# Kernel optimization log

Hardware: AMD Instinct MI355X
Metric: run time of the kernel (lower is better)

## Reference

```python
import jax, jax.numpy as jnp
import numpy as np

E = 100000   # num edges
N = 50000    # num nodes (eg_idx, v, t triples)
B = 64       # num queries / subgraphs
D = 128      # n_dims_in
ID = 4 * D   # concat of 4 embeddings
OD = 2 * D   # G output dims
K = 1000     # max_edges per eg_idx


def setup_inputs() -> dict:
    key = jax.random.key(0)
    ks = jax.random.split(key, 12)
    eg_idx = jnp.sort(jax.random.randint(ks[0], (E,), 0, B)).astype(jnp.int32)
    node_i = jax.random.randint(ks[1], (E,), 0, N).astype(jnp.int32)
    node_j = jax.random.randint(ks[2], (E,), 0, N).astype(jnp.int32)
    node_score = jax.random.uniform(ks[3], (N,), dtype=jnp.float32)
    memorized_embedding = jax.random.normal(ks[4], (N, D), dtype=jnp.float32)
    rel_emb = jax.random.normal(ks[5], (E, D), dtype=jnp.float32)
    query_src_ts_emb = jax.random.normal(ks[6], (B, D), dtype=jnp.float32)
    query_rel_emb = jax.random.normal(ks[7], (B, D), dtype=jnp.float32)
    # G params: left/right dense init ~ N(0, sqrt(2/in)), center xavier-ish
    Wl = jax.random.normal(ks[8], (ID, OD), dtype=jnp.float32) * np.sqrt(2.0 / ID)
    Wr = jax.random.normal(ks[9], (ID, OD), dtype=jnp.float32) * np.sqrt(2.0 / ID)
    Wc = jax.random.normal(ks[10], (OD, OD), dtype=jnp.float32) * np.sqrt(2.0 / (OD + OD))
    bl = jnp.zeros((OD,), jnp.float32)
    br = jnp.zeros((OD,), jnp.float32)
    bc = jnp.zeros((OD,), jnp.float32)
    return dict(eg_idx=eg_idx, node_i=node_i, node_j=node_j, node_score=node_score,
                memorized_embedding=memorized_embedding, rel_emb=rel_emb,
                query_src_ts_emb=query_src_ts_emb, query_rel_emb=query_rel_emb,
                Wl=Wl, bl=bl, Wr=Wr, br=br, Wc=Wc, bc=bc, k=K)


def _segment_softmax(logits, seg, num_segments):
    m = jax.ops.segment_max(logits, seg, num_segments=num_segments)
    e = jnp.exp(logits - m[seg])
    s = jax.ops.segment_sum(e, seg, num_segments=num_segments)
    return e / s[seg]


def _topk_keep_mask(scores, group, num_groups, k):
    # keep edge iff its score ranks < k within its group (per-eg_idx topk)
    n = scores.shape[0]
    order = jnp.lexsort((-scores, group))          # sort by group asc, score desc
    sorted_group = group[order]
    counts = jax.ops.segment_sum(jnp.ones((n,), jnp.int32), group, num_segments=num_groups)
    starts = jnp.cumsum(counts) - counts           # exclusive cumsum: group start offsets
    rank_in_group = jnp.arange(n) - starts[sorted_group]
    keep_sorted = rank_in_group < k
    return jnp.zeros((n,), bool).at[order].set(keep_sorted)


def reference(eg_idx, node_i, node_j, node_score, memorized_embedding, rel_emb,
              query_src_ts_emb, query_rel_emb, Wl, bl, Wr, br, Wc, bc, k):
    num_nodes = memorized_embedding.shape[0]
    num_groups = query_src_ts_emb.shape[0]
    # gather per-edge embeddings
    hvi = memorized_embedding[node_i]              # [E, D]
    hvj = memorized_embedding[node_j]
    q_src = query_src_ts_emb[eg_idx]               # [E, D]
    q_rel = query_rel_emb[eg_idx]
    # G: bilinear MLP attention
    left_x = jnp.concatenate([hvi, rel_emb, q_src, q_rel], axis=-1)   # [E, 4D]
    right_x = jnp.concatenate([hvj, rel_emb, q_src, q_rel], axis=-1)
    l = jax.nn.leaky_relu(left_x @ Wl + bl)                           # [E, 2D]
    r = jax.nn.leaky_relu(right_x @ Wr + br) @ Wc + bc
    transition_logits = jnp.sum(l * r, axis=-1)                       # [E]
    # segment softmax over source node (eg_idx, vi, ti)
    soft = _segment_softmax(transition_logits, node_i, num_nodes)
    src_att = node_score[node_i]
    target_att = soft * src_att
    # per-eg_idx top-k pruning (keep mask instead of ragged slicing)
    keep = _topk_keep_mask(target_att, eg_idx, num_groups, k).astype(target_att.dtype)
    # sum aggregation: scatter soft * target_att into target nodes over kept edges
    updated_node_score = jax.ops.segment_sum(keep * soft * target_att, node_j,
                                             num_segments=num_nodes)
    return updated_node_score
```

## Files before the change

### kernel.cpp

```cpp
#include <hip/hip_runtime.h>

#define DD   128
#define ODIM 256
#define TE   32
#define TSLICE 16

__device__ __forceinline__ float leaky(float v) { return v > 0.f ? v : 0.01f * v; }

__global__ void k_query(const float* __restrict__ qs, const float* __restrict__ qr,
                        const float* __restrict__ Wl, const float* __restrict__ bl,
                        const float* __restrict__ Wr, const float* __restrict__ br,
                        float* __restrict__ Ql, float* __restrict__ Qr)
{
    const int g = blockIdx.x, t = threadIdx.x;
    float al = bl[t], ar = br[t];
    const float* qsg = qs + (size_t)g * DD;
    const float* qrg = qr + (size_t)g * DD;
    for (int k = 0; k < DD; ++k) {
        float a = qsg[k], b = qrg[k];
        al = fmaf(a, Wl[(size_t)(256 + k) * ODIM + t], al);
        al = fmaf(b, Wl[(size_t)(384 + k) * ODIM + t], al);
        ar = fmaf(a, Wr[(size_t)(256 + k) * ODIM + t], ar);
        ar = fmaf(b, Wr[(size_t)(384 + k) * ODIM + t], ar);
    }
    Ql[(size_t)g * ODIM + t] = al;
    Qr[(size_t)g * ODIM + t] = ar;
}

#define FMA4(dst, xc, wv, j)                                \
    dst[j][0] = fmaf(xc, wv.x, dst[j][0]);                  \
    dst[j][1] = fmaf(xc, wv.y, dst[j][1]);                  \
    dst[j][2] = fmaf(xc, wv.z, dst[j][2]);                  \
    dst[j][3] = fmaf(xc, wv.w, dst[j][3]);

__global__ __launch_bounds__(256, 2)
void k_nodepre(const float* __restrict__ me, const float* __restrict__ Wl,
               const float* __restrict__ Wr, float* __restrict__ Xl,
               float* __restrict__ Xr, int N)
{
    __shared__ float s_me[TE][DD];

    const int tx = threadIdx.x;
    const int cg = tx & 63;
    const int er = tx >> 6;
    const int c0 = cg << 2;
    const int n0 = blockIdx.x * TE;
    const int eb = er * 8;

    for (int it = tx; it < TE * DD / 4; it += 256) {
        int i  = it >> 5;
        int kk = (it & 31) << 2;
        float4 h = make_float4(0.f, 0.f, 0.f, 0.f);
        if (n0 + i < N) h = *(const float4*)(me + (size_t)(n0 + i) * DD + kk);
        *(float4*)(&s_me[i][kk]) = h;
    }
    __syncthreads();

    float acc[8][4];
#pragma unroll
    for (int j = 0; j < 8; ++j) { acc[j][0] = acc[j][1] = acc[j][2] = acc[j][3] = 0.f; }
#pragma unroll 2
    for (int k = 0; k < DD; k += 4) {
        const float* wp = Wl + (size_t)k * ODIM + c0;
        float4 w0 = *(const float4*)(wp);
        float4 w1 = *(const float4*)(wp + ODIM);
        float4 w2 = *(const float4*)(wp + 2 * ODIM);
        float4 w3 = *(const float4*)(wp + 3 * ODIM);
#pragma unroll
        for (int j = 0; j < 8; ++j) {
            float4 x = *(const float4*)(&s_me[eb + j][k]);
            FMA4(acc, x.x, w0, j) FMA4(acc, x.y, w1, j) FMA4(acc, x.z, w2, j) FMA4(acc, x.w, w3, j)
        }
    }
#pragma unroll
    for (int j = 0; j < 8; ++j) {
        int n = n0 + eb + j;
        if (n < N)
            *(float4*)(Xl + (size_t)n * ODIM + c0) = make_float4(acc[j][0], acc[j][1], acc[j][2], acc[j][3]);
    }

#pragma unroll
    for (int j = 0; j < 8; ++j) { acc[j][0] = acc[j][1] = acc[j][2] = acc[j][3] = 0.f; }
#pragma unroll 2
    for (int k = 0; k < DD; k += 4) {
        const float* wp = Wr + (size_t)k * ODIM + c0;
        float4 w0 = *(const float4*)(wp);
        float4 w1 = *(const float4*)(wp + ODIM);
        float4 w2 = *(const float4*)(wp + 2 * ODIM);
        float4 w3 = *(const float4*)(wp + 3 * ODIM);
#pragma unroll
        for (int j = 0; j < 8; ++j) {
            float4 x = *(const float4*)(&s_me[eb + j][k]);
            FMA4(acc, x.x, w0, j) FMA4(acc, x.y, w1, j) FMA4(acc, x.z, w2, j) FMA4(acc, x.w, w3, j)
        }
    }
#pragma unroll
    for (int j = 0; j < 8; ++j) {
        int n = n0 + eb + j;
        if (n < N)
            *(float4*)(Xr + (size_t)n * ODIM + c0) = make_float4(acc[j][0], acc[j][1], acc[j][2], acc[j][3]);
    }
}

__global__ __launch_bounds__(256, 2)
void k_edge_logits_pre(const int* __restrict__ eg_idx, const int* __restrict__ node_i,
                       const int* __restrict__ node_j, const float* __restrict__ rel,
                       const float* __restrict__ Wl, const float* __restrict__ Wr,
                       const float* __restrict__ Wc, const float* __restrict__ bc,
                       const float* __restrict__ Ql, const float* __restrict__ Qr,
                       const float* __restrict__ Xl, const float* __restrict__ Xr,
                       float* __restrict__ logits, int E)
{
    __shared__ float s_a[TE][DD];
    __shared__ float s_b[TE][DD];
    __shared__ int   s_ni[TE], s_nj[TE], s_g[TE];

    const int tx = threadIdx.x;
    const int cg = tx & 63;
    const int er = tx >> 6;
    const int c0 = cg << 2;
    const int e0 = blockIdx.x * TE;
    const int eb = er * 8;

    if (tx < TE) {
        int e = e0 + tx;
        s_ni[tx] = (e < E) ? node_i[e] : 0;
        s_nj[tx] = (e < E) ? node_j[e] : 0;
        s_g[tx]  = (e < E) ? eg_idx[e] : 0;
    }
    __syncthreads();

    for (int it = tx; it < TE * DD / 4; it += 256) {
        int i  = it >> 5;
        int kk = (it & 31) << 2;
        float4 v = make_float4(0.f, 0.f, 0.f, 0.f);
        if (e0 + i < E) v = *(const float4*)(rel + (size_t)(e0 + i) * DD + kk);
        *(float4*)(&s_a[i][kk]) = v;
    }
    __syncthreads();

    float acc[8][4];
#pragma unroll
    for (int j = 0; j < 8; ++j) { acc[j][0] = acc[j][1] = acc[j][2] = acc[j][3] = 0.f; }

#pragma unroll 2
    for (int k = 0; k < DD; k += 4) {
        const float* wp = Wr + (size_t)(DD + k) * ODIM + c0;
        float4 w0 = *(const float4*)(wp);
        float4 w1 = *(const float4*)(wp + ODIM);
        float4 w2 = *(const float4*)(wp + 2 * ODIM);
        float4 w3 = *(const float4*)(wp + 3 * ODIM);
#pragma unroll
        for (int j = 0; j < 8; ++j) {
            float4 x = *(const float4*)(&s_a[eb + j][k]);
            FMA4(acc, x.x, w0, j) FMA4(acc, x.y, w1, j) FMA4(acc, x.z, w2, j) FMA4(acc, x.w, w3, j)
        }
    }

#pragma unroll
    for (int j = 0; j < 8; ++j) {
        float4 xr = *(const float4*)(Xr + (size_t)s_nj[eb + j] * ODIM + c0);
        float4 q  = *(const float4*)(Qr + (size_t)s_g[eb + j] * ODIM + c0);
        acc[j][0] = leaky(acc[j][0] + xr.x + q.x);
        acc[j][1] = leaky(acc[j][1] + xr.y + q.y);
        acc[j][2] = leaky(acc[j][2] + xr.z + q.z);
        acc[j][3] = leaky(acc[j][3] + xr.w + q.w);
    }

    float uacc[8][4];
#pragma unroll
    for (int j = 0; j < 8; ++j) { uacc[j][0] = uacc[j][1] = uacc[j][2] = uacc[j][3] = 0.f; }

    if (c0 < DD) {
#pragma unroll
        for (int j = 0; j < 8; ++j)
            *(float4*)(&s_b[eb + j][c0]) = make_float4(acc[j][0], acc[j][1], acc[j][2], acc[j][3]);
    }
    __syncthreads();
#pragma unroll 2
    for (int k = 0; k < DD; k += 4) {
        const float* wp = Wc + (size_t)k * ODIM + c0;
        float4 w0 = *(const float4*)(wp);
        float4 w1 = *(const float4*)(wp + ODIM);
        float4 w2 = *(const float4*)(wp + 2 * ODIM);
        float4 w3 = *(const float4*)(wp + 3 * ODIM);
#pragma unroll
        for (int j = 0; j < 8; ++j) {
            float4 x = *(const float4*)(&s_b[eb + j][k]);
            FMA4(uacc, x.x, w0, j) FMA4(uacc, x.y, w1, j) FMA4(uacc, x.z, w2, j) FMA4(uacc, x.w, w3, j)
        }
    }
    __syncthreads();
    if (c0 >= DD) {
#pragma unroll
        for (int j = 0; j < 8; ++j)
            *(float4*)(&s_b[eb + j][c0 - DD]) = make_float4(acc[j][0], acc[j][1], acc[j][2], acc[j][3]);
    }
    __syncthreads();
#pragma unroll 2
    for (int k = 0; k < DD; k += 4) {
        const float* wp = Wc + (size_t)(DD + k) * ODIM + c0;
        float4 w0 = *(const float4*)(wp);
        float4 w1 = *(const float4*)(wp + ODIM);
        float4 w2 = *(const float4*)(wp + 2 * ODIM);
        float4 w3 = *(const float4*)(wp + 3 * ODIM);
#pragma unroll
        for (int j = 0; j < 8; ++j) {
            float4 x = *(const float4*)(&s_b[eb + j][k]);
            FMA4(uacc, x.x, w0, j) FMA4(uacc, x.y, w1, j) FMA4(uacc, x.z, w2, j) FMA4(uacc, x.w, w3, j)
        }
    }

    {
        float4 bcv = *(const float4*)(bc + c0);
#pragma unroll
        for (int j = 0; j < 8; ++j) {
            uacc[j][0] += bcv.x; uacc[j][1] += bcv.y;
            uacc[j][2] += bcv.z; uacc[j][3] += bcv.w;
        }
    }

#pragma unroll
    for (int j = 0; j < 8; ++j) { acc[j][0] = acc[j][1] = acc[j][2] = acc[j][3] = 0.f; }
#pragma unroll 2
    for (int k = 0; k < DD; k += 4) {
        const float* wp = Wl + (size_t)(DD + k) * ODIM + c0;
        float4 w0 = *(const float4*)(wp);
        float4 w1 = *(const float4*)(wp + ODIM);
        float4 w2 = *(const float4*)(wp + 2 * ODIM);
        float4 w3 = *(const float4*)(wp + 3 * ODIM);
#pragma unroll
        for (int j = 0; j < 8; ++j) {
            float4 x = *(const float4*)(&s_a[eb + j][k]);
            FMA4(acc, x.x, w0, j) FMA4(acc, x.y, w1, j) FMA4(acc, x.z, w2, j) FMA4(acc, x.w, w3, j)
        }
    }

#pragma unroll
    for (int j = 0; j < 8; ++j) {
        float4 xl = *(const float4*)(Xl + (size_t)s_ni[eb + j] * ODIM + c0);
        float4 q  = *(const float4*)(Ql + (size_t)s_g[eb + j] * ODIM + c0);
        float p = leaky(acc[j][0] + xl.x + q.x) * uacc[j][0]
                + leaky(acc[j][1] + xl.y + q.y) * uacc[j][1]
                + leaky(acc[j][2] + xl.z + q.z) * uacc[j][2]
                + leaky(acc[j][3] + xl.w + q.w) * uacc[j][3];
#pragma unroll
        for (int off = 32; off > 0; off >>= 1) p += __shfl_down(p, off);
        if (cg == 0) {
            int e = e0 + eb + j;
            if (e < E) logits[e] = p;
        }
    }
}

__global__ __launch_bounds__(256, 2)
void k_edge_logits(const int* __restrict__ eg_idx, const int* __restrict__ node_i,
                   const int* __restrict__ node_j,
                   const float* __restrict__ me, const float* __restrict__ rel,
                   const float* __restrict__ Wl, const float* __restrict__ Wr,
                   const float* __restrict__ Wc, const float* __restrict__ bc,
                   const float* __restrict__ Ql, const float* __restrict__ Qr,
                   float* __restrict__ logits, int E)
{
    __shared__ float s_a[TE][DD];
    __shared__ float s_b[TE][DD];
    __shared__ int   s_ni[TE], s_nj[TE], s_g[TE];

    const int tx = threadIdx.x;
    const int cg = tx & 63;
    const int er = tx >> 6;
    const int c0 = cg << 2;
    const int e0 = blockIdx.x * TE;
    const int eb = er * 8;

    if (tx < TE) {
        int e = e0 + tx;
        s_ni[tx] = (e < E) ? node_i[e] : 0;
        s_nj[tx] = (e < E) ? node_j[e] : 0;
        s_g[tx]  = (e < E) ? eg_idx[e] : 0;
    }
    __syncthreads();

    for (int it = tx; it < TE * DD / 4; it += 256) {
        int i  = it >> 5;
        int kk = (it & 31) << 2;
        float4 v = make_float4(0.f, 0.f, 0.f, 0.f);
        float4 h = v;
        if (e0 + i < E) {
            v = *(const float4*)(rel + (size_t)(e0 + i) * DD + kk);
            h = *(const float4*)(me + (size_t)s_nj[i] * DD + kk);
        }
        *(float4*)(&s_a[i][kk]) = v;
        *(float4*)(&s_b[i][kk]) = h;
    }
    __syncthreads();

    float acc[8][4];
#pragma unroll
    for (int j = 0; j < 8; ++j) { acc[j][0] = acc[j][1] = acc[j][2] = acc[j][3] = 0.f; }

    for (int k = 0; k < DD; k += 4) {
        const float* wp = Wr + (size_t)k * ODIM + c0;
        float4 w0 = *(const float4*)(wp);
        float4 w1 = *(const float4*)(wp + ODIM);
        float4 w2 = *(const float4*)(wp + 2 * ODIM);
        float4 w3 = *(const float4*)(wp + 3 * ODIM);
#pragma unroll
        for (int j = 0; j < 8; ++j) {
            float4 x = *(const float4*)(&s_b[eb + j][k]);
            FMA4(acc, x.x, w0, j) FMA4(acc, x.y, w1, j) FMA4(acc, x.z, w2, j) FMA4(acc, x.w, w3, j)
        }
    }
    for (int k = 0; k < DD; k += 4) {
        const float* wp = Wr + (size_t)(DD + k) * ODIM + c0;
        float4 w0 = *(const float4*)(wp);
        float4 w1 = *(const float4*)(wp + ODIM);
        float4 w2 = *(const float4*)(wp + 2 * ODIM);
        float4 w3 = *(const float4*)(wp + 3 * ODIM);
#pragma unroll
        for (int j = 0; j < 8; ++j) {
            float4 x = *(const float4*)(&s_a[eb + j][k]);
            FMA4(acc, x.x, w0, j) FMA4(acc, x.y, w1, j) FMA4(acc, x.z, w2, j) FMA4(acc, x.w, w3, j)
        }
    }

#pragma unroll
    for (int j = 0; j < 8; ++j) {
        int g = s_g[eb + j];
        float4 q = *(const float4*)(Qr + (size_t)g * ODIM + c0);
        acc[j][0] = leaky(acc[j][0] + q.x);
        acc[j][1] = leaky(acc[j][1] + q.y);
        acc[j][2] = leaky(acc[j][2] + q.z);
        acc[j][3] = leaky(acc[j][3] + q.w);
    }

    float uacc[8][4];
#pragma unroll
    for (int j = 0; j < 8; ++j) { uacc[j][0] = uacc[j][1] = uacc[j][2] = uacc[j][3] = 0.f; }

    __syncthreads();
    if (c0 < DD) {
#pragma unroll
        for (int j = 0; j < 8; ++j)
            *(float4*)(&s_b[eb + j][c0]) = make_float4(acc[j][0], acc[j][1], acc[j][2], acc[j][3]);
    }
    __syncthreads();
    for (int k = 0; k < DD; k += 4) {
        const float* wp = Wc + (size_t)k * ODIM + c0;
        float4 w0 = *(const float4*)(wp);
        float4 w1 = *(const float4*)(wp + ODIM);
        float4 w2 = *(const float4*)(wp + 2 * ODIM);
        float4 w3 = *(const float4*)(wp + 3 * ODIM);
#pragma unroll
        for (int j = 0; j < 8; ++j) {
            float4 x = *(const float4*)(&s_b[eb + j][k]);
            FMA4(uacc, x.x, w0, j) FMA4(uacc, x.y, w1, j) FMA4(uacc, x.z, w2, j) FMA4(uacc, x.w, w3, j)
        }
    }
    __syncthreads();
    if (c0 >= DD) {
#pragma unroll
        for (int j = 0; j < 8; ++j)
            *(float4*)(&s_b[eb + j][c0 - DD]) = make_float4(acc[j][0], acc[j][1], acc[j][2], acc[j][3]);
    }
    __syncthreads();
    for (int k = 0; k < DD; k += 4) {
        const float* wp = Wc + (size_t)(DD + k) * ODIM + c0;
        float4 w0 = *(const float4*)(wp);
        float4 w1 = *(const float4*)(wp + ODIM);
        float4 w2 = *(const float4*)(wp + 2 * ODIM);
        float4 w3 = *(const float4*)(wp + 3 * ODIM);
#pragma unroll
        for (int j = 0; j < 8; ++j) {
            float4 x = *(const float4*)(&s_b[eb + j][k]);
            FMA4(uacc, x.x, w0, j) FMA4(uacc, x.y, w1, j) FMA4(uacc, x.z, w2, j) FMA4(uacc, x.w, w3, j)
        }
    }

    {
        float4 bcv = *(const float4*)(bc + c0);
#pragma unroll
        for (int j = 0; j < 8; ++j) {
            uacc[j][0] += bcv.x; uacc[j][1] += bcv.y;
            uacc[j][2] += bcv.z; uacc[j][3] += bcv.w;
        }
    }

    __syncthreads();
    for (int it = tx; it < TE * DD / 4; it += 256) {
        int i  = it >> 5;
        int kk = (it & 31) << 2;
        float4 h = make_float4(0.f, 0.f, 0.f, 0.f);
        if (e0 + i < E) h = *(const float4*)(me + (size_t)s_ni[i] * DD + kk);
        *(float4*)(&s_b[i][kk]) = h;
    }
    __syncthreads();

#pragma unroll
    for (int j = 0; j < 8; ++j) { acc[j][0] = acc[j][1] = acc[j][2] = acc[j][3] = 0.f; }

    for (int k = 0; k < DD; k += 4) {
        const float* wp = Wl + (size_t)k * ODIM + c0;
        float4 w0 = *(const float4*)(wp);
        float4 w1 = *(const float4*)(wp + ODIM);
        float4 w2 = *(const float4*)(wp + 2 * ODIM);
        float4 w3 = *(const float4*)(wp + 3 * ODIM);
#pragma unroll
        for (int j = 0; j < 8; ++j) {
            float4 x = *(const float4*)(&s_b[eb + j][k]);
            FMA4(acc, x.x, w0, j) FMA4(acc, x.y, w1, j) FMA4(acc, x.z, w2, j) FMA4(acc, x.w, w3, j)
        }
    }
    for (int k = 0; k < DD; k += 4) {
        const float* wp = Wl + (size_t)(DD + k) * ODIM + c0;
        float4 w0 = *(const float4*)(wp);
        float4 w1 = *(const float4*)(wp + ODIM);
        float4 w2 = *(const float4*)(wp + 2 * ODIM);
        float4 w3 = *(const float4*)(wp + 3 * ODIM);
#pragma unroll
        for (int j = 0; j < 8; ++j) {
            float4 x = *(const float4*)(&s_a[eb + j][k]);
            FMA4(acc, x.x, w0, j) FMA4(acc, x.y, w1, j) FMA4(acc, x.z, w2, j) FMA4(acc, x.w, w3, j)
        }
    }

#pragma unroll
    for (int j = 0; j < 8; ++j) {
        int g = s_g[eb + j];
        float4 q = *(const float4*)(Ql + (size_t)g * ODIM + c0);
        float p = leaky(acc[j][0] + q.x) * uacc[j][0]
                + leaky(acc[j][1] + q.y) * uacc[j][1]
                + leaky(acc[j][2] + q.z) * uacc[j][2]
                + leaky(acc[j][3] + q.w) * uacc[j][3];
#pragma unroll
        for (int off = 32; off > 0; off >>= 1) p += __shfl_down(p, off);
        if (cg == 0) {
            int e = e0 + eb + j;
            if (e < E) logits[e] = p;
        }
    }
}

__device__ __forceinline__ unsigned f32_enc(float f) {
    unsigned u = __float_as_uint(f);
    return (u & 0x80000000u) ? ~u : (u | 0x80000000u);
}
__device__ __forceinline__ float f32_dec(unsigned x) {
    return (x & 0x80000000u) ? __uint_as_float(x & 0x7fffffffu) : __uint_as_float(~x);
}

__global__ void k_segmax(const float* __restrict__ logits, const int* __restrict__ ni,
                         unsigned* __restrict__ segmax, int E)
{
    int e = blockIdx.x * 256 + threadIdx.x;
    if (e >= E) return;
    atomicMax(&segmax[ni[e]], f32_enc(logits[e]));
}

__global__ void k_expsum(const float* __restrict__ logits, const int* __restrict__ ni,
                         const unsigned* __restrict__ segmax,
                         float* __restrict__ eexp, float* __restrict__ segsum, int E)
{
    int e = blockIdx.x * 256 + threadIdx.x;
    if (e >= E) return;
    float m = f32_dec(segmax[ni[e]]);
    float v = expf(logits[e] - m);
    eexp[e] = v;
    atomicAdd(&segsum[ni[e]], v);
}

__global__ void k_soft(const float* __restrict__ eexp, const float* __restrict__ segsum,
                       const int* __restrict__ ni, const float* __restrict__ node_score,
                       float* __restrict__ soft, float* __restrict__ ta, int E)
{
    int e = blockIdx.x * 256 + threadIdx.x;
    if (e >= E) return;
    int n = ni[e];
    float s = eexp[e] / segsum[n];
    soft[e] = s;
    ta[e]   = s * node_score[n];
}

__global__ void k_starts(const int* __restrict__ eg, int E, int B, int* __restrict__ starts)
{
    int g = blockIdx.x * blockDim.x + threadIdx.x;
    if (g > B) return;
    int lo = 0, hi = E;
    while (lo < hi) { int mid = (lo + hi) >> 1; if (eg[mid] < g) lo = mid + 1; else hi = mid; }
    starts[g] = lo;
}

__global__ __launch_bounds__(256)
void k_topk(const int* __restrict__ starts, const int* __restrict__ node_j,
            const float* __restrict__ soft, const float* __restrict__ ta,
            const int* __restrict__ kptr, float* __restrict__ out)
{
    __shared__ float s_val[2048];
    const int g  = blockIdx.x / TSLICE;
    const int sl = blockIdx.x % TSLICE;
    const int gs = starts[g], ge = starts[g + 1];
    const int cnt = ge - gs;
    if (cnt <= 0) return;
    const int per = (cnt + TSLICE - 1) / TSLICE;
    const int c0  = sl * per;
    const int c1  = min(cnt, c0 + per);
    if (c0 >= cnt) return;
    const int K  = kptr[0];
    const int tx = threadIdx.x;

    for (int base = c0; base < c1; base += 256) {
        int   li  = base + tx;
        bool  act = li < c1;
        float mv  = act ? ta[gs + li] : 0.f;
        int   rank = 0;
        for (int t0 = 0; t0 < cnt; t0 += 2048) {
            int tlen = min(2048, cnt - t0);
            __syncthreads();
            for (int i = tx; i < tlen; i += 256) s_val[i] = ta[gs + t0 + i];
            __syncthreads();
            for (int i = 0; i < tlen; ++i) {
                float v  = s_val[i];
                int   gi = t0 + i;
                rank += (int)((v > mv) || (v == mv && gi < li));
            }
        }
        if (act && rank < K) {
            int e = gs + li;
            atomicAdd(&out[node_j[e]], soft[e] * ta[e]);
        }
    }
}

extern "C" void kernel_launch(void* const* d_in, const int* in_sizes, int n_in,
                              void* d_out, int out_size, void* d_ws, size_t ws_size,
                              hipStream_t stream)
{
    const int*   eg_idx     = (const int*)d_in[0];
    const int*   node_i     = (const int*)d_in[1];
    const int*   node_j     = (const int*)d_in[2];
    const float* node_score = (const float*)d_in[3];
    const float* me         = (const float*)d_in[4];
    const float* rel        = (const float*)d_in[5];
    const float* qs         = (const float*)d_in[6];
    const float* qr         = (const float*)d_in[7];
    const float* Wl         = (const float*)d_in[8];
    const float* bl         = (const float*)d_in[9];
    const float* Wr         = (const float*)d_in[10];
    const float* br         = (const float*)d_in[11];
    const float* Wc         = (const float*)d_in[12];
    const float* bc         = (const float*)d_in[13];
    const int*   kptr       = (const int*)d_in[14];

    const int E = in_sizes[0];
    const int N = in_sizes[3];
    const int B = in_sizes[6] / DD;

    float* ws      = (float*)d_ws;
    float* logits  = ws;
    float* eexp    = ws + (size_t)E;
    float* soft    = ws + 2 * (size_t)E;
    float* ta      = ws + 3 * (size_t)E;
    unsigned* segmax = (unsigned*)(ws + 4 * (size_t)E);
    float* segsum  = ws + 4 * (size_t)E + (size_t)N;
    float* Ql      = ws + 4 * (size_t)E + 2 * (size_t)N;
    float* Qr      = Ql + (size_t)B * ODIM;
    int*   starts  = (int*)(Qr + (size_t)B * ODIM);
    size_t base    = 4 * (size_t)E + 2 * (size_t)N + 2 * (size_t)B * ODIM + (size_t)(B + 1);
    float* Xl      = ws + base;
    float* Xr      = Xl + (size_t)N * ODIM;
    size_t needed  = (base + 2 * (size_t)N * ODIM) * sizeof(float);
    bool use_pre   = ws_size >= needed;

    hipMemsetAsync(d_out, 0, (size_t)N * sizeof(float), stream);
    hipMemsetAsync(segmax, 0, (size_t)2 * N * sizeof(float), stream);

    k_query<<<B, 256, 0, stream>>>(qs, qr, Wl, bl, Wr, br, Ql, Qr);
    if (use_pre) {
        k_nodepre<<<(N + TE - 1) / TE, 256, 0, stream>>>(me, Wl, Wr, Xl, Xr, N);
        k_edge_logits_pre<<<(E + TE - 1) / TE, 256, 0, stream>>>(eg_idx, node_i, node_j, rel,
                                                                 Wl, Wr, Wc, bc, Ql, Qr,
                                                                 Xl, Xr, logits, E);
    } else {
        k_edge_logits<<<(E + TE - 1) / TE, 256, 0, stream>>>(eg_idx, node_i, node_j, me, rel,
                                                             Wl, Wr, Wc, bc, Ql, Qr, logits, E);
    }
    int gE = (E + 255) / 256;
    k_segmax<<<gE, 256, 0, stream>>>(logits, node_i, segmax, E);
    k_expsum<<<gE, 256, 0, stream>>>(logits, node_i, segmax, eexp, segsum, E);
    k_soft<<<gE, 256, 0, stream>>>(eexp, segsum, node_i, node_score, soft, ta, E);
    k_starts<<<1, 128, 0, stream>>>(eg_idx, E, B, starts);
    k_topk<<<B * TSLICE, 256, 0, stream>>>(starts, node_j, soft, ta, kptr, (float*)d_out);
}
```

Before: 630.0 us.

## Remap threads so each wave owns a column slice across all tile edges

Changes the thread-to-work mapping in the node-precompute and edge-logit GEMM kernels. Each wave now covers a 64-column slice for all 32 edges instead of all 256 columns for 8 edges, so weight float4 loads per wave shrink and LDS reads of the activation tile become more broadcast-friendly. The per-edge dot-product reduction now uses a 16-lane xor shuffle plus a small shared-memory cross-wave sum. The partial unroll pragmas are also removed. The trade-off is an extra barrier and LDS buffer, and a possible change in register pressure.

```diff
diff --git a/kernel.cpp b/kernel.cpp
--- a/kernel.cpp
+++ b/kernel.cpp
@@ -33,6 +33,7 @@
     dst[j][2] = fmaf(xc, wv.z, dst[j][2]);                  \
     dst[j][3] = fmaf(xc, wv.w, dst[j][3]);
 
+
 __global__ __launch_bounds__(256, 2)
 void k_nodepre(const float* __restrict__ me, const float* __restrict__ Wl,
                const float* __restrict__ Wr, float* __restrict__ Xl,
@@ -40,12 +41,14 @@
 {
     __shared__ float s_me[TE][DD];
 
-    const int tx = threadIdx.x;
-    const int cg = tx & 63;
-    const int er = tx >> 6;
-    const int c0 = cg << 2;
-    const int n0 = blockIdx.x * TE;
-    const int eb = er * 8;
+    const int tx   = threadIdx.x;
+    const int wave = tx >> 6;
+    const int lane = tx & 63;
+    const int colg = lane & 15;
+    const int edgeg= lane >> 4;
+    const int c0   = wave * 64 + colg * 4;
+    const int eb   = edgeg * 8;
+    const int n0   = blockIdx.x * TE;
 
     for (int it = tx; it < TE * DD / 4; it += 256) {
         int i  = it >> 5;
@@ -59,7 +62,6 @@
     float acc[8][4];
 #pragma unroll
     for (int j = 0; j < 8; ++j) { acc[j][0] = acc[j][1] = acc[j][2] = acc[j][3] = 0.f; }
-#pragma unroll 2
     for (int k = 0; k < DD; k += 4) {
         const float* wp = Wl + (size_t)k * ODIM + c0;
         float4 w0 = *(const float4*)(wp);
@@ -81,7 +83,6 @@
 
 #pragma unroll
     for (int j = 0; j < 8; ++j) { acc[j][0] = acc[j][1] = acc[j][2] = acc[j][3] = 0.f; }
-#pragma unroll 2
     for (int k = 0; k < DD; k += 4) {
         const float* wp = Wr + (size_t)k * ODIM + c0;
         float4 w0 = *(const float4*)(wp);
@@ -113,14 +114,17 @@
 {
     __shared__ float s_a[TE][DD];
     __shared__ float s_b[TE][DD];
+    __shared__ float s_red[4][TE];
     __shared__ int   s_ni[TE], s_nj[TE], s_g[TE];
 
-    const int tx = threadIdx.x;
-    const int cg = tx & 63;
-    const int er = tx >> 6;
-    const int c0 = cg << 2;
-    const int e0 = blockIdx.x * TE;
-    const int eb = er * 8;
+    const int tx   = threadIdx.x;
+    const int wave = tx >> 6;
+    const int lane = tx & 63;
+    const int colg = lane & 15;
+    const int edgeg= lane >> 4;
+    const int c0   = wave * 64 + colg * 4;
+    const int eb   = edgeg * 8;
+    const int e0   = blockIdx.x * TE;
 
     if (tx < TE) {
         int e = e0 + tx;
@@ -143,7 +147,6 @@
 #pragma unroll
     for (int j = 0; j < 8; ++j) { acc[j][0] = acc[j][1] = acc[j][2] = acc[j][3] = 0.f; }
 
-#pragma unroll 2
     for (int k = 0; k < DD; k += 4) {
         const float* wp = Wr + (size_t)(DD + k) * ODIM + c0;
         float4 w0 = *(const float4*)(wp);
@@ -171,13 +174,12 @@
 #pragma unroll
     for (int j = 0; j < 8; ++j) { uacc[j][0] = uacc[j][1] = uacc[j][2] = uacc[j][3] = 0.f; }
 
-    if (c0 < DD) {
+    if (wave < 2) {
 #pragma unroll
         for (int j = 0; j < 8; ++j)
             *(float4*)(&s_b[eb + j][c0]) = make_float4(acc[j][0], acc[j][1], acc[j][2], acc[j][3]);
     }
     __syncthreads();
-#pragma unroll 2
     for (int k = 0; k < DD; k += 4) {
         const float* wp = Wc + (size_t)k * ODIM + c0;
         float4 w0 = *(const float4*)(wp);
@@ -191,13 +193,12 @@
         }
     }
     __syncthreads();
-    if (c0 >= DD) {
+    if (wave >= 2) {
 #pragma unroll
         for (int j = 0; j < 8; ++j)
             *(float4*)(&s_b[eb + j][c0 - DD]) = make_float4(acc[j][0], acc[j][1], acc[j][2], acc[j][3]);
     }
     __syncthreads();
-#pragma unroll 2
     for (int k = 0; k < DD; k += 4) {
         const float* wp = Wc + (size_t)(DD + k) * ODIM + c0;
         float4 w0 = *(const float4*)(wp);
@@ -222,7 +223,6 @@
 
 #pragma unroll
     for (int j = 0; j < 8; ++j) { acc[j][0] = acc[j][1] = acc[j][2] = acc[j][3] = 0.f; }
-#pragma unroll 2
     for (int k = 0; k < DD; k += 4) {
         const float* wp = Wl + (size_t)(DD + k) * ODIM + c0;
         float4 w0 = *(const float4*)(wp);
@@ -244,12 +244,17 @@
                 + leaky(acc[j][1] + xl.y + q.y) * uacc[j][1]
                 + leaky(acc[j][2] + xl.z + q.z) * uacc[j][2]
                 + leaky(acc[j][3] + xl.w + q.w) * uacc[j][3];
-#pragma unroll
-        for (int off = 32; off > 0; off >>= 1) p += __shfl_down(p, off);
-        if (cg == 0) {
-            int e = e0 + eb + j;
-            if (e < E) logits[e] = p;
-        }
+        p += __shfl_xor(p, 1);
+        p += __shfl_xor(p, 2);
+        p += __shfl_xor(p, 4);
+        p += __shfl_xor(p, 8);
+        if (colg == 0) s_red[wave][eb + j] = p;
+    }
+    __syncthreads();
+    if (tx < TE) {
+        int e = e0 + tx;
+        if (e < E)
+            logits[e] = s_red[0][tx] + s_red[1][tx] + s_red[2][tx] + s_red[3][tx];
     }
 }
 
```

Measured after the change: 581.3 us. 7.7% less time.

## Double-buffer weight chunks into LDS via async global_load_lds in GEMM kernels

Applied to the files above, without the earlier changes.

Instead of each thread reading weight float4s straight from global memory inside the k-loop, weights are staged in 8-row chunks into a double-buffered LDS tile using __builtin_amdgcn_global_load_lds. The next chunk is prefetched while the current one is consumed, with one barrier per chunk. This targets global-load latency and redundant per-wave weight fetches in the node-precompute and edge-logit kernels. The cost is extra LDS (16 KB), a __syncthreads per chunk, and reliance on the barrier to cover async LDS-write completion. The fallback kernel only has TE replaced by the literal 32.

```diff
diff --git a/kernel.cpp b/kernel.cpp
--- a/kernel.cpp
+++ b/kernel.cpp
@@ -1,9 +1,13 @@
 #include <hip/hip_runtime.h>
 
-#define DD   128
-#define ODIM 256
-#define TE   32
+#define DD     128
+#define ODIM   256
+#define TE     32
+#define WCHUNK 8
 #define TSLICE 16
+
+#define GLOBAL_AS __attribute__((address_space(1)))
+#define LDS_AS    __attribute__((address_space(3)))
 
 __device__ __forceinline__ float leaky(float v) { return v > 0.f ? v : 0.01f * v; }
 
@@ -33,19 +37,54 @@
     dst[j][2] = fmaf(xc, wv.z, dst[j][2]);                  \
     dst[j][3] = fmaf(xc, wv.w, dst[j][3]);
 
+#define GEMM_CHUNK(XS, DST)                                              \
+    {                                                                    \
+        _Pragma("unroll")                                                \
+        for (int kk = 0; kk < 2; ++kk) {                                 \
+            const int k = cbase + kk * 4;                                \
+            float4 w0 = *(const float4*)(&s_w[buf][kk * 4 + 0][c0]);     \
+            float4 w1 = *(const float4*)(&s_w[buf][kk * 4 + 1][c0]);     \
+            float4 w2 = *(const float4*)(&s_w[buf][kk * 4 + 2][c0]);     \
+            float4 w3 = *(const float4*)(&s_w[buf][kk * 4 + 3][c0]);     \
+            _Pragma("unroll")                                            \
+            for (int j = 0; j < 8; ++j) {                                \
+                float4 x = *(const float4*)(&XS[eb + j][k]);             \
+                FMA4(DST, x.x, w0, j) FMA4(DST, x.y, w1, j)              \
+                FMA4(DST, x.z, w2, j) FMA4(DST, x.w, w3, j)              \
+            }                                                            \
+        }                                                                \
+    }
+
 __global__ __launch_bounds__(256, 2)
 void k_nodepre(const float* __restrict__ me, const float* __restrict__ Wl,
                const float* __restrict__ Wr, float* __restrict__ Xl,
                float* __restrict__ Xr, int N)
 {
     __shared__ float s_me[TE][DD];
-
-    const int tx = threadIdx.x;
-    const int cg = tx & 63;
-    const int er = tx >> 6;
-    const int c0 = cg << 2;
-    const int n0 = blockIdx.x * TE;
-    const int eb = er * 8;
+    __shared__ float s_w[2][WCHUNK][ODIM];
+
+    const int tx   = threadIdx.x;
+    const int cg   = tx & 63;
+    const int er   = tx >> 6;
+    const int lane = cg;
+    const int c0   = cg << 2;
+    const int eb   = er * 8;
+    const int n0   = blockIdx.x * TE;
+
+    auto wseq = [&](int c) -> const float* {
+        return (c < 16) ? (Wl + (size_t)(8 * c) * ODIM)
+                        : (Wr + (size_t)(8 * (c - 16)) * ODIM);
+    };
+    auto stage_w = [&](const float* base, int nb) {
+#pragma unroll
+        for (int q = 0; q < 2; ++q) {
+            int off = er * 512 + q * 256 + lane * 4;
+            __builtin_amdgcn_global_load_lds(
+                (const GLOBAL_AS void*)(base + off),
+                (LDS_AS void*)(&s_w[nb][0][0] + off),
+                16, 0, 0);
+        }
+    };
 
     for (int it = tx; it < TE * DD / 4; it += 256) {
         int i  = it >> 5;
@@ -54,23 +93,20 @@
         if (n0 + i < N) h = *(const float4*)(me + (size_t)(n0 + i) * DD + kk);
         *(float4*)(&s_me[i][kk]) = h;
     }
+    stage_w(wseq(0), 0);
     __syncthreads();
 
     float acc[8][4];
 #pragma unroll
     for (int j = 0; j < 8; ++j) { acc[j][0] = acc[j][1] = acc[j][2] = acc[j][3] = 0.f; }
-#pragma unroll 2
-    for (int k = 0; k < DD; k += 4) {
-        const float* wp = Wl + (size_t)k * ODIM + c0;
-        float4 w0 = *(const float4*)(wp);
-        float4 w1 = *(const float4*)(wp + ODIM);
-        float4 w2 = *(const float4*)(wp + 2 * ODIM);
-        float4 w3 = *(const float4*)(wp + 3 * ODIM);
-#pragma unroll
-        for (int j = 0; j < 8; ++j) {
-            float4 x = *(const float4*)(&s_me[eb + j][k]);
-            FMA4(acc, x.x, w0, j) FMA4(acc, x.y, w1, j) FMA4(acc, x.z, w2, j) FMA4(acc, x.w, w3, j)
-        }
+    int buf = 0;
+
+    for (int c = 0; c < 16; ++c) {
+        stage_w(wseq(c + 1), buf ^ 1);
+        const int cbase = c * 8;
+        GEMM_CHUNK(s_me, acc)
+        __syncthreads();
+        buf ^= 1;
     }
 #pragma unroll
     for (int j = 0; j < 8; ++j) {
@@ -81,18 +117,13 @@
 
 #pragma unroll
     for (int j = 0; j < 8; ++j) { acc[j][0] = acc[j][1] = acc[j][2] = acc[j][3] = 0.f; }
-#pragma unroll 2
-    for (int k = 0; k < DD; k += 4) {
-        const float* wp = Wr + (size_t)k * ODIM + c0;
-        float4 w0 = *(const float4*)(wp);
-        float4 w1 = *(const float4*)(wp + ODIM);
-        float4 w2 = *(const float4*)(wp + 2 * ODIM);
-        float4 w3 = *(const float4*)(wp + 3 * ODIM);
-#pragma unroll
-        for (int j = 0; j < 8; ++j) {
-            float4 x = *(const float4*)(&s_me[eb + j][k]);
-            FMA4(acc, x.x, w0, j) FMA4(acc, x.y, w1, j) FMA4(acc, x.z, w2, j) FMA4(acc, x.w, w3, j)
-        }
+
+    for (int c = 16; c < 32; ++c) {
+        if (c < 31) stage_w(wseq(c + 1), buf ^ 1);
+        const int cbase = (c - 16) * 8;
+        GEMM_CHUNK(s_me, acc)
+        __syncthreads();
+        buf ^= 1;
     }
 #pragma unroll
     for (int j = 0; j < 8; ++j) {
@@ -113,14 +144,33 @@
 {
     __shared__ float s_a[TE][DD];
     __shared__ float s_b[TE][DD];
+    __shared__ float s_w[2][WCHUNK][ODIM];
     __shared__ int   s_ni[TE], s_nj[TE], s_g[TE];
 
-    const int tx = threadIdx.x;
-    const int cg = tx & 63;
-    const int er = tx >> 6;
-    const int c0 = cg << 2;
-    const int e0 = blockIdx.x * TE;
-    const int eb = er * 8;
+    const int tx   = threadIdx.x;
+    const int cg   = tx & 63;
+    const int er   = tx >> 6;
+    const int lane = cg;
+    const int c0   = cg << 2;
+    const int e0   = blockIdx.x * TE;
+    const int eb   = er * 8;
+
+    auto wseq = [&](int c) -> const float* {
+        if (c < 16) return Wr + (size_t)(DD + 8 * c) * ODIM;
+        if (c < 32) return Wc + (size_t)(8 * (c - 16)) * ODIM;
+        if (c < 48) return Wc + (size_t)(DD + 8 * (c - 32)) * ODIM;
+        return Wl + (size_t)(DD + 8 * (c - 48)) * ODIM;
+    };
+    auto stage_w = [&](const float* base, int nb) {
+#pragma unroll
+        for (int q = 0; q < 2; ++q) {
+            int off = er * 512 + q * 256 + lane * 4;
+            __builtin_amdgcn_global_load_lds(
+                (const GLOBAL_AS void*)(base + off),
+                (LDS_AS void*)(&s_w[nb][0][0] + off),
+                16, 0, 0);
+        }
+    };
 
     if (tx < TE) {
         int e = e0 + tx;
@@ -128,7 +178,6 @@
         s_nj[tx] = (e < E) ? node_j[e] : 0;
         s_g[tx]  = (e < E) ? eg_idx[e] : 0;
     }
-    __syncthreads();
 
     for (int it = tx; it < TE * DD / 4; it += 256) {
         int i  = it >> 5;
@@ -137,24 +186,20 @@
         if (e0 + i < E) v = *(const float4*)(rel + (size_t)(e0 + i) * DD + kk);
         *(float4*)(&s_a[i][kk]) = v;
     }
+    stage_w(wseq(0), 0);
     __syncthreads();
 
     float acc[8][4];
 #pragma unroll
     for (int j = 0; j < 8; ++j) { acc[j][0] = acc[j][1] = acc[j][2] = acc[j][3] = 0.f; }
-
-#pragma unroll 2
-    for (int k = 0; k < DD; k += 4) {
-        const float* wp = Wr + (size_t)(DD + k) * ODIM + c0;
-        float4 w0 = *(const float4*)(wp);
-        float4 w1 = *(const float4*)(wp + ODIM);
-        float4 w2 = *(const float4*)(wp + 2 * ODIM);
-        float4 w3 = *(const float4*)(wp + 3 * ODIM);
-#pragma unroll
-        for (int j = 0; j < 8; ++j) {
-            float4 x = *(const float4*)(&s_a[eb + j][k]);
-            FMA4(acc, x.x, w0, j) FMA4(acc, x.y, w1, j) FMA4(acc, x.z, w2, j) FMA4(acc, x.w, w3, j)
-        }
+    int buf = 0;
+
+    for (int c = 0; c < 16; ++c) {
+        stage_w(wseq(c + 1), buf ^ 1);
+        const int cbase = c * 8;
+        GEMM_CHUNK(s_a, acc)
+        __syncthreads();
+        buf ^= 1;
     }
 
 #pragma unroll
@@ -177,38 +222,28 @@
             *(float4*)(&s_b[eb + j][c0]) = make_float4(acc[j][0], acc[j][1], acc[j][2], acc[j][3]);
     }
     __syncthreads();
-#pragma unroll 2
-    for (int k = 0; k < DD; k += 4) {
-        const float* wp = Wc + (size_t)k * ODIM + c0;
-        float4 w0 = *(const float4*)(wp);
-        float4 w1 = *(const float4*)(wp + ODIM);
-        float4 w2 = *(const float4*)(wp + 2 * ODIM);
-        float4 w3 = *(const float4*)(wp + 3 * ODIM);
-#pragma unroll
-        for (int j = 0; j < 8; ++j) {
-            float4 x = *(const float4*)(&s_b[eb + j][k]);
-            FMA4(uacc, x.x, w0, j) FMA4(uacc, x.y, w1, j) FMA4(uacc, x.z, w2, j) FMA4(uacc, x.w, w3, j)
-        }
-    }
-    __syncthreads();
+
+    for (int c = 16; c < 32; ++c) {
+        stage_w(wseq(c + 1), buf ^ 1);
+        const int cbase = (c - 16) * 8;
+        GEMM_CHUNK(s_b, uacc)
+        __syncthreads();
+        buf ^= 1;
+    }
+
     if (c0 >= DD) {
 #pragma unroll
         for (int j = 0; j < 8; ++j)
             *(float4*)(&s_b[eb + j][c0 - DD]) = make_float4(acc[j][0], acc[j][1], acc[j][2], acc[j][3]);
     }
     __syncthreads();
-#pragma unroll 2
-    for (int k = 0; k < DD; k += 4) {
-        const float* wp = Wc + (size_t)(DD + k) * ODIM + c0;
-        float4 w0 = *(const float4*)(wp);
-        float4 w1 = *(const float4*)(wp + ODIM);
-        float4 w2 = *(const float4*)(wp + 2 * ODIM);
-        float4 w3 = *(const float4*)(wp + 3 * ODIM);
-#pragma unroll
-        for (int j = 0; j < 8; ++j) {
-            float4 x = *(const float4*)(&s_b[eb + j][k]);
-            FMA4(uacc, x.x, w0, j) FMA4(uacc, x.y, w1, j) FMA4(uacc, x.z, w2, j) FMA4(uacc, x.w, w3, j)
-        }
+
+    for (int c = 32; c < 48; ++c) {
+        stage_w(wseq(c + 1), buf ^ 1);
+        const int cbase = (c - 32) * 8;
+        GEMM_CHUNK(s_b, uacc)
+        __syncthreads();
+        buf ^= 1;
     }
 
     {
@@ -222,18 +257,12 @@
 
 #pragma unroll
     for (int j = 0; j < 8; ++j) { acc[j][0] = acc[j][1] = acc[j][2] = acc[j][3] = 0.f; }
-#pragma unroll 2
-    for (int k = 0; k < DD; k += 4) {
-        const float* wp = Wl + (size_t)(DD + k) * ODIM + c0;
-        float4 w0 = *(const float4*)(wp);
-        float4 w1 = *(const float4*)(wp + ODIM);
-        float4 w2 = *(const float4*)(wp + 2 * ODIM);
-        float4 w3 = *(const float4*)(wp + 3 * ODIM);
-#pragma unroll
-        for (int j = 0; j < 8; ++j) {
-            float4 x = *(const float4*)(&s_a[eb + j][k]);
-            FMA4(acc, x.x, w0, j) FMA4(acc, x.y, w1, j) FMA4(acc, x.z, w2, j) FMA4(acc, x.w, w3, j)
-        }
+    for (int c = 48; c < 64; ++c) {
+        if (c < 63) stage_w(wseq(c + 1), buf ^ 1);
+        const int cbase = (c - 48) * 8;
+        GEMM_CHUNK(s_a, acc)
+        __syncthreads();
+        buf ^= 1;
     }
 
 #pragma unroll
@@ -262,18 +291,18 @@
                    const float* __restrict__ Ql, const float* __restrict__ Qr,
                    float* __restrict__ logits, int E)
 {
-    __shared__ float s_a[TE][DD];
-    __shared__ float s_b[TE][DD];
-    __shared__ int   s_ni[TE], s_nj[TE], s_g[TE];
+    __shared__ float s_a[32][DD];
+    __shared__ float s_b[32][DD];
+    __shared__ int   s_ni[32], s_nj[32], s_g[32];
 
     const int tx = threadIdx.x;
     const int cg = tx & 63;
     const int er = tx >> 6;
     const int c0 = cg << 2;
-    const int e0 = blockIdx.x * TE;
+    const int e0 = blockIdx.x * 32;
     const int eb = er * 8;
 
-    if (tx < TE) {
+    if (tx < 32) {
         int e = e0 + tx;
         s_ni[tx] = (e < E) ? node_i[e] : 0;
         s_nj[tx] = (e < E) ? node_j[e] : 0;
@@ -281,7 +310,7 @@
     }
     __syncthreads();
 
-    for (int it = tx; it < TE * DD / 4; it += 256) {
+    for (int it = tx; it < 32 * DD / 4; it += 256) {
         int i  = it >> 5;
         int kk = (it & 31) << 2;
         float4 v = make_float4(0.f, 0.f, 0.f, 0.f);
@@ -387,7 +416,7 @@
     }
 
     __syncthreads();
-    for (int it = tx; it < TE * DD / 4; it += 256) {
+    for (int it = tx; it < 32 * DD / 4; it += 256) {
         int i  = it >> 5;
         int kk = (it & 31) << 2;
         float4 h = make_float4(0.f, 0.f, 0.f, 0.f);
@@ -581,8 +610,8 @@
                                                                  Wl, Wr, Wc, bc, Ql, Qr,
                                                                  Xl, Xr, logits, E);
     } else {
-        k_edge_logits<<<(E + TE - 1) / TE, 256, 0, stream>>>(eg_idx, node_i, node_j, me, rel,
-                                                             Wl, Wr, Wc, bc, Ql, Qr, logits, E);
+        k_edge_logits<<<(E + 31) / 32, 256, 0, stream>>>(eg_idx, node_i, node_j, me, rel,
+                                                         Wl, Wr, Wc, bc, Ql, Qr, logits, E);
     }
     int gE = (E + 255) / 256;
     k_segmax<<<gE, 256, 0, stream>>>(logits, node_i, segmax, E);
```

Result: slower. 659.0 us (+4.6%).
